# Optimization experiments

Measured on AMD Instinct MI355X. Metric: run time of the kernel, lower is better.

## Reference

```python
import jax, jax.numpy as jnp
import numpy as np

B, T, H, NSPK = 8, 1024, 1024, 2
LN_EPS = 1e-5


def setup_inputs() -> dict:
    key = jax.random.key(0)
    ks = jax.random.split(key, 12)
    s = 1.0 / np.sqrt(H)
    return {
        "x": jax.random.normal(ks[0], (B, T, H), jnp.float32),
        "qmask": jax.random.uniform(ks[1], (B, T, NSPK), jnp.float32),
        "dia_len": jax.random.randint(ks[2], (B,), T // 2, T + 1),
        "wp": 8,
        "wf": 8,
        "W_msg": jax.random.normal(ks[3], (H, H), jnp.float32) * s,
        "b_msg": jax.random.normal(ks[4], (H,), jnp.float32) * s,
        "W_self": jax.random.normal(ks[5], (H, H), jnp.float32) * s,
        "b_self": jax.random.normal(ks[6], (H,), jnp.float32) * s,
        "W_out": jax.random.normal(ks[7], (H, H), jnp.float32) * s,
        "b_out": jax.random.normal(ks[8], (H,), jnp.float32) * s,
        "gamma": jnp.ones((H,), jnp.float32),
        "beta": jnp.zeros((H,), jnp.float32),
    }


def reference(x, qmask, dia_len, wp, wf, W_msg, b_msg, W_self, b_self, W_out, b_out, gamma, beta):
    Bb, Tt, Hh = x.shape
    spk = jnp.argmax(qmask, axis=-1)                     # [B,T]
    pos = jnp.arange(Tt)
    offs = jnp.arange(-wp, wf + 1)                       # [W]
    idx = pos[:, None] + offs[None, :]                   # [T,W] window indices
    vlen = dia_len[:, None, None]                        # [B,1,1]
    valid = (idx[None] >= 0) & (idx[None] <= vlen - 1)   # [B,T,W]
    idxc = jnp.clip(idx, 0, Tt - 1)
    nb = jnp.take(x, idxc, axis=1)                       # [B,T,W,H]
    nb_spk = jnp.take(spk, idxc, axis=1)                 # [B,T,W]
    same = (nb_spk == spk[:, :, None]).astype(x.dtype)
    w = jnp.where(valid, 0.5 + 0.5 * same, 0.0)          # speaker weights, masked
    cnt = jnp.maximum(valid.sum(-1).astype(x.dtype), 1.0)  # window sizes [B,T]
    msg = jnp.einsum('btw,btwh->bth', w, nb) / cnt[..., None]
    h = x @ W_self + b_self + msg @ W_msg + b_msg        # per-node fusion
    node_valid = (pos[None, :] < dia_len[:, None])[..., None]
    out = jnp.where(node_valid, h, x)                    # nodes past dia_len keep x
    y = jax.nn.relu(out) @ W_out + b_out                 # dropout = identity (eval)
    z = x + y
    mean = z.mean(-1, keepdims=True)
    var = z.var(-1, keepdims=True)
    return gamma * (z - mean) / jnp.sqrt(var + LN_EPS) + beta
```

## Files before the change

### kernel.cpp

```cpp
#include <hip/hip_runtime.h>


typedef unsigned short u16;
typedef float floatx4 __attribute__((ext_vector_type(4)));
typedef short shortx8 __attribute__((ext_vector_type(8)));

#define T_ 1024
#define H_ 1024

__device__ __forceinline__ float bf2f(u16 v) {
    return __uint_as_float(((unsigned)v) << 16);
}
__device__ __forceinline__ u16 f2bf(float f) {
    unsigned u = __float_as_uint(f);
    return (u16)((u + 0x7fffu + ((u >> 16) & 1u)) >> 16);
}
__device__ __forceinline__ void async16(const void* g, void* l) {
    __builtin_amdgcn_global_load_lds(
        (__attribute__((address_space(1))) void*)g,
        (__attribute__((address_space(3))) void*)l, 16, 0, 0);
}

__global__ __launch_bounds__(256)
void pack_x(const float* __restrict__ x, u16* __restrict__ xbf)
{
    const size_t i = ((size_t)blockIdx.x * 256 + threadIdx.x) * 4;
    float4 v = *(const float4*)(x + i);
    ushort4 o;
    o.x = f2bf(v.x); o.y = f2bf(v.y); o.z = f2bf(v.z); o.w = f2bf(v.w);
    *(ushort4*)(xbf + i) = o;
}

__global__ __launch_bounds__(256)
void transpose_pack(const float* __restrict__ Wself, const float* __restrict__ Wmsg,
                    const float* __restrict__ Wout,
                    u16* __restrict__ wt1, u16* __restrict__ wt_out)
{
    __shared__ float s[32][33];
    const int wid = blockIdx.z;
    const float* src = (wid == 0) ? Wself : ((wid == 1) ? Wmsg : Wout);
    const int n0 = blockIdx.x * 32, k0 = blockIdx.y * 32;
    const int tx = threadIdx.x & 31, ty = threadIdx.x >> 5;
#pragma unroll
    for (int i = 0; i < 4; ++i) {
        int k = k0 + ty + 8 * i;
        s[ty + 8 * i][tx] = src[(size_t)k * H_ + n0 + tx];
    }
    __syncthreads();
#pragma unroll
    for (int i = 0; i < 4; ++i) {
        int n = n0 + ty + 8 * i;
        u16 v = f2bf(s[tx][ty + 8 * i]);
        if (wid == 0)      wt1[(size_t)n * 1024 + k0 + tx] = v;
        else if (wid == 1) wt1[(size_t)(n + 1024) * 1024 + k0 + tx] = v;
        else               wt_out[(size_t)n * 1024 + k0 + tx] = v;
    }
}

template <int KLEN, int EPI>
__global__ __launch_bounds__(256)
void gemm_bt(const u16* __restrict__ A, const u16* __restrict__ Bt,
             u16* __restrict__ O0, u16* __restrict__ O1)
{
    __shared__ u16 smem[2 * 8192];
    const int tid = threadIdx.x;
    const int bn = blockIdx.x * 128;
    const int bm = blockIdx.y * 128;
    const int kb = blockIdx.z * KLEN;
    const int wave = tid >> 6, lane = tid & 63;
    const int wr = wave >> 1, wc = wave & 1;
    const int lrow = lane & 15, lq = lane >> 4;

    const u16* gA0 = A + (size_t)(bm + (tid >> 2)) * 1024 + kb + (tid & 3) * 8;
    const u16* gA1 = gA0 + (size_t)64 * 1024;
    const u16* gB0 = Bt + (size_t)(bn + (tid >> 2)) * 1024 + kb + (tid & 3) * 8;
    const u16* gB1 = gB0 + (size_t)64 * 1024;

    floatx4 acc[4][4];
#pragma unroll
    for (int i = 0; i < 4; ++i)
#pragma unroll
        for (int j = 0; j < 4; ++j)
            acc[i][j] = (floatx4){0.f, 0.f, 0.f, 0.f};

    const int aoff = (wr * 64 + lrow) * 32 + lq * 8;
    const int boff = 4096 + (wc * 64 + lrow) * 32 + lq * 8;

    auto issue = [&](int s, int p) {
        u16* base = smem + p * 8192 + wave * 512;
        const int k = s * 32;
        async16(gA0 + k, base);
        async16(gA1 + k, base + 2048);
        async16(gB0 + k, base + 4096);
        async16(gB1 + k, base + 4096 + 2048);
    };

    constexpr int NS = KLEN / 32;
    issue(0, 0);
#pragma unroll 2
    for (int s = 0; s < NS; ++s) {
        const int p = s & 1;
        if (s + 1 < NS) {
            issue(s + 1, p ^ 1);
            asm volatile("s_waitcnt vmcnt(4)" ::: "memory");
        } else {
            asm volatile("s_waitcnt vmcnt(0)" ::: "memory");
        }
        asm volatile("s_barrier" ::: "memory");
        const u16* pa = smem + p * 8192 + aoff;
        const u16* pb = smem + p * 8192 + boff;
        shortx8 av[4], bv[4];
#pragma unroll
        for (int i = 0; i < 4; ++i) av[i] = *(const shortx8*)(pa + i * 512);
#pragma unroll
        for (int j = 0; j < 4; ++j) bv[j] = *(const shortx8*)(pb + j * 512);
#pragma unroll
        for (int i = 0; i < 4; ++i)
#pragma unroll
            for (int j = 0; j < 4; ++j)
                acc[i][j] = __builtin_amdgcn_mfma_f32_16x16x32_bf16(
                    av[i], bv[j], acc[i][j], 0, 0, 0);
        asm volatile("s_barrier" ::: "memory");
    }

    u16* O;
    int cbase;
    if (EPI == 0) { O = (bn < 1024) ? O0 : O1; cbase = bn & 1023; }
    else          { O = blockIdx.z ? O1 : O0;  cbase = bn; }
#pragma unroll
    for (int i = 0; i < 4; ++i) {
        const int row0 = bm + wr * 64 + i * 16 + lq * 4;
#pragma unroll
        for (int j = 0; j < 4; ++j) {
            const int col = cbase + wc * 64 + j * 16 + lrow;
#pragma unroll
            for (int r = 0; r < 4; ++r)
                O[(size_t)(row0 + r) * 1024 + col] = f2bf(acc[i][j][r]);
        }
    }
}

__global__ __launch_bounds__(256)
void combine(u16* uv, const u16* __restrict__ v,
             const float* __restrict__ x, const float* __restrict__ qmask,
             const int* __restrict__ dia_len, const float* __restrict__ b_self,
             const float* __restrict__ b_msg)
{
    __shared__ u16 sv[32][1024];
    const int tid = threadIdx.x;
    const int b = blockIdx.y;
    const int t0 = blockIdx.x * 16;
    const int dlen = dia_len[b];
    const int c4 = tid * 4;

    unsigned spkmask = 0;
#pragma unroll 4
    for (int rr = 0; rr < 32; ++rr) {
        int row = t0 - 8 + rr;
        row = row < 0 ? 0 : (row > T_ - 1 ? T_ - 1 : row);
        const float* q = qmask + ((size_t)b * T_ + row) * 2;
        spkmask |= (q[1] > q[0] ? 1u : 0u) << rr;
        *(ushort4*)&sv[rr][c4] =
            *(const ushort4*)(v + ((size_t)b * T_ + row) * 1024 + c4);
    }
    __syncthreads();

    float4 bs;
    {
        float4 b1 = *(const float4*)(b_self + c4);
        float4 b2 = *(const float4*)(b_msg + c4);
        bs.x = b1.x + b2.x; bs.y = b1.y + b2.y;
        bs.z = b1.z + b2.z; bs.w = b1.w + b2.w;
    }

    for (int lt = 0; lt < 16; ++lt) {
        const int t = t0 + lt;
        const unsigned cs = (spkmask >> (lt + 8)) & 1u;
        float a0 = 0.f, a1 = 0.f, a2 = 0.f, a3 = 0.f;
        int cnt = 0;
#pragma unroll
        for (int o = 0; o < 17; ++o) {
            const int idx = t + o - 8;
            if (idx >= 0 && idx < dlen) {
                const float w = (((spkmask >> (lt + o)) & 1u) == cs) ? 1.0f : 0.5f;
                ++cnt;
                ushort4 uu = *(const ushort4*)&sv[lt + o][c4];
                a0 += w * bf2f(uu.x); a1 += w * bf2f(uu.y);
                a2 += w * bf2f(uu.z); a3 += w * bf2f(uu.w);
            }
        }
        const float inv = 1.0f / (float)(cnt > 0 ? cnt : 1);
        const size_t rowg = (size_t)b * T_ + t;
        ushort4 u4 = *(const ushort4*)(uv + rowg * 1024 + c4);
        float4 xv = *(const float4*)(x + rowg * H_ + c4);
        const bool sel = (t < dlen);
        float h0 = bf2f(u4.x) + bs.x + a0 * inv;
        float h1 = bf2f(u4.y) + bs.y + a1 * inv;
        float h2 = bf2f(u4.z) + bs.z + a2 * inv;
        float h3 = bf2f(u4.w) + bs.w + a3 * inv;
        ushort4 outv;
        outv.x = f2bf(fmaxf(sel ? h0 : xv.x, 0.f));
        outv.y = f2bf(fmaxf(sel ? h1 : xv.y, 0.f));
        outv.z = f2bf(fmaxf(sel ? h2 : xv.z, 0.f));
        outv.w = f2bf(fmaxf(sel ? h3 : xv.w, 0.f));
        *(ushort4*)(uv + rowg * 1024 + c4) = outv;
    }
}

__global__ __launch_bounds__(256)
void ln_final(const u16* __restrict__ P0, const u16* __restrict__ P1,
              const float* __restrict__ x, const float* __restrict__ b_out,
              const float* __restrict__ gamma, const float* __restrict__ beta,
              float* __restrict__ out)
{
    const int row = blockIdx.x;
    const int tid = threadIdx.x;
    const size_t base = (size_t)row * H_ + tid * 4;
    float4 xv = *(const float4*)(x + base);
    ushort4 p0 = *(const ushort4*)(P0 + base);
    ushort4 p1 = *(const ushort4*)(P1 + base);
    float4 bo = *(const float4*)(b_out + tid * 4);
    float4 v;
    v.x = xv.x + bf2f(p0.x) + bf2f(p1.x) + bo.x;
    v.y = xv.y + bf2f(p0.y) + bf2f(p1.y) + bo.y;
    v.z = xv.z + bf2f(p0.z) + bf2f(p1.z) + bo.z;
    v.w = xv.w + bf2f(p0.w) + bf2f(p1.w) + bo.w;
    float s = v.x + v.y + v.z + v.w;
    float q = v.x * v.x + v.y * v.y + v.z * v.z + v.w * v.w;
#pragma unroll
    for (int off = 32; off > 0; off >>= 1) {
        s += __shfl_down(s, off);
        q += __shfl_down(q, off);
    }
    __shared__ float ps[4], pq[4];
    const int wave = tid >> 6, lane = tid & 63;
    if (lane == 0) { ps[wave] = s; pq[wave] = q; }
    __syncthreads();
    const float S = ps[0] + ps[1] + ps[2] + ps[3];
    const float Q = pq[0] + pq[1] + pq[2] + pq[3];
    const float mean = S * (1.0f / 1024.0f);
    const float var = Q * (1.0f / 1024.0f) - mean * mean;
    const float inv = rsqrtf(var + 1e-5f);
    float4 g = *(const float4*)(gamma + tid * 4);
    float4 bt = *(const float4*)(beta + tid * 4);
    float4 o;
    o.x = g.x * (v.x - mean) * inv + bt.x;
    o.y = g.y * (v.y - mean) * inv + bt.y;
    o.z = g.z * (v.z - mean) * inv + bt.z;
    o.w = g.w * (v.w - mean) * inv + bt.w;
    *(float4*)(out + base) = o;
}

extern "C" void kernel_launch(void* const* d_in, const int* in_sizes, int n_in,
                              void* d_out, int out_size, void* d_ws, size_t ws_size,
                              hipStream_t stream)
{
    (void)in_sizes; (void)n_in; (void)out_size; (void)ws_size;
    const float* x       = (const float*)d_in[0];
    const float* qmask   = (const float*)d_in[1];
    const int*   dia_len = (const int*)d_in[2];
    const float* W_msg   = (const float*)d_in[5];
    const float* b_msg   = (const float*)d_in[6];
    const float* W_self  = (const float*)d_in[7];
    const float* b_self  = (const float*)d_in[8];
    const float* W_out   = (const float*)d_in[9];
    const float* b_out   = (const float*)d_in[10];
    const float* gamma   = (const float*)d_in[11];
    const float* beta    = (const float*)d_in[12];
    float* out = (float*)d_out;

    char* ws = (char*)d_ws;
    u16* region0 = (u16*)ws;
    u16* region1 = (u16*)(ws + (size_t)(16u << 20));
    u16* region2 = (u16*)(ws + (size_t)(32u << 20));
    u16* wt1     = (u16*)(ws + (size_t)(48u << 20));
    u16* wt_out  = (u16*)(ws + (size_t)(52u << 20));

    pack_x<<<dim3(8192), 256, 0, stream>>>(x, region0);
    transpose_pack<<<dim3(32, 32, 3), 256, 0, stream>>>(W_self, W_msg, W_out,
                                                        wt1, wt_out);
    gemm_bt<1024, 0><<<dim3(16, 64, 1), 256, 0, stream>>>(region0, wt1,
                                                          region1, region2);
    combine<<<dim3(64, 8), 256, 0, stream>>>(region1, region2, x, qmask,
                                             dia_len, b_self, b_msg);
    gemm_bt<512, 1><<<dim3(8, 64, 2), 256, 0, stream>>>(region1, wt_out,
                                                        region2, region0);
    ln_final<<<dim3(8192), 256, 0, stream>>>(region2, region0, x, b_out,
                                             gamma, beta, out);
}
```

Measured before the change: 234.5 us.

## Merge prep kernels, load GEMM B operand directly to registers, simplify combine

Fuses the x bf16 pack and weight transpose into a single prep launch to cut one launch. The GEMM now loads B fragments straight from global memory into double-buffered registers instead of staging them through LDS, which halves shared memory and removes the LDS reads for B. The cost is uncoalesced per-lane global loads with no reuse across waves. The combine kernel becomes one row per block, reading the 17 neighbour rows from global/L2 instead of staging a 32-row tile in shared memory. That removes LDS pressure but raises global traffic roughly 17x for v.

```diff
diff --git a/kernel.cpp b/kernel.cpp
--- a/kernel.cpp
+++ b/kernel.cpp
@@ -22,38 +22,41 @@
 }
 
 __global__ __launch_bounds__(256)
-void pack_x(const float* __restrict__ x, u16* __restrict__ xbf)
-{
-    const size_t i = ((size_t)blockIdx.x * 256 + threadIdx.x) * 4;
-    float4 v = *(const float4*)(x + i);
-    ushort4 o;
-    o.x = f2bf(v.x); o.y = f2bf(v.y); o.z = f2bf(v.z); o.w = f2bf(v.w);
-    *(ushort4*)(xbf + i) = o;
-}
-
-__global__ __launch_bounds__(256)
-void transpose_pack(const float* __restrict__ Wself, const float* __restrict__ Wmsg,
-                    const float* __restrict__ Wout,
-                    u16* __restrict__ wt1, u16* __restrict__ wt_out)
+void prep(const float* __restrict__ Wself, const float* __restrict__ Wmsg,
+          const float* __restrict__ Wout, const float* __restrict__ x,
+          u16* __restrict__ wt1, u16* __restrict__ wt_out, u16* __restrict__ xbf)
 {
     __shared__ float s[32][33];
-    const int wid = blockIdx.z;
-    const float* src = (wid == 0) ? Wself : ((wid == 1) ? Wmsg : Wout);
-    const int n0 = blockIdx.x * 32, k0 = blockIdx.y * 32;
-    const int tx = threadIdx.x & 31, ty = threadIdx.x >> 5;
-#pragma unroll
-    for (int i = 0; i < 4; ++i) {
-        int k = k0 + ty + 8 * i;
-        s[ty + 8 * i][tx] = src[(size_t)k * H_ + n0 + tx];
-    }
-    __syncthreads();
-#pragma unroll
-    for (int i = 0; i < 4; ++i) {
-        int n = n0 + ty + 8 * i;
-        u16 v = f2bf(s[tx][ty + 8 * i]);
-        if (wid == 0)      wt1[(size_t)n * 1024 + k0 + tx] = v;
-        else if (wid == 1) wt1[(size_t)(n + 1024) * 1024 + k0 + tx] = v;
-        else               wt_out[(size_t)n * 1024 + k0 + tx] = v;
+    const int bid = blockIdx.x;
+    if (bid < 3072) {
+        const int wid = bid >> 10;
+        const int rem = bid & 1023;
+        const float* src = (wid == 0) ? Wself : ((wid == 1) ? Wmsg : Wout);
+        const int n0 = (rem & 31) * 32, k0 = (rem >> 5) * 32;
+        const int tx = threadIdx.x & 31, ty = threadIdx.x >> 5;
+#pragma unroll
+        for (int i = 0; i < 4; ++i) {
+            int k = k0 + ty + 8 * i;
+            s[ty + 8 * i][tx] = src[(size_t)k * H_ + n0 + tx];
+        }
+        __syncthreads();
+#pragma unroll
+        for (int i = 0; i < 4; ++i) {
+            int n = n0 + ty + 8 * i;
+            u16 v = f2bf(s[tx][ty + 8 * i]);
+            if (wid == 0)      wt1[(size_t)n * 1024 + k0 + tx] = v;
+            else if (wid == 1) wt1[(size_t)(n + 1024) * 1024 + k0 + tx] = v;
+            else               wt_out[(size_t)n * 1024 + k0 + tx] = v;
+        }
+    } else {
+        const size_t i = ((size_t)(bid - 3072) * 256 + threadIdx.x) * 8;
+        float4 v0 = *(const float4*)(x + i);
+        float4 v1 = *(const float4*)(x + i + 4);
+        ushort4 o0, o1;
+        o0.x = f2bf(v0.x); o0.y = f2bf(v0.y); o0.z = f2bf(v0.z); o0.w = f2bf(v0.w);
+        o1.x = f2bf(v1.x); o1.y = f2bf(v1.y); o1.z = f2bf(v1.z); o1.w = f2bf(v1.w);
+        *(ushort4*)(xbf + i) = o0;
+        *(ushort4*)(xbf + i + 4) = o1;
     }
 }
 
@@ -62,7 +65,7 @@
 void gemm_bt(const u16* __restrict__ A, const u16* __restrict__ Bt,
              u16* __restrict__ O0, u16* __restrict__ O1)
 {
-    __shared__ u16 smem[2 * 8192];
+    __shared__ u16 sA[2][4096];
     const int tid = threadIdx.x;
     const int bn = blockIdx.x * 128;
     const int bm = blockIdx.y * 128;
@@ -73,8 +76,7 @@
 
     const u16* gA0 = A + (size_t)(bm + (tid >> 2)) * 1024 + kb + (tid & 3) * 8;
     const u16* gA1 = gA0 + (size_t)64 * 1024;
-    const u16* gB0 = Bt + (size_t)(bn + (tid >> 2)) * 1024 + kb + (tid & 3) * 8;
-    const u16* gB1 = gB0 + (size_t)64 * 1024;
+    const u16* gB = Bt + (size_t)(bn + wc * 64 + lrow) * 1024 + kb + lq * 8;
 
     floatx4 acc[4][4];
 #pragma unroll
@@ -84,42 +86,45 @@
             acc[i][j] = (floatx4){0.f, 0.f, 0.f, 0.f};
 
     const int aoff = (wr * 64 + lrow) * 32 + lq * 8;
-    const int boff = 4096 + (wc * 64 + lrow) * 32 + lq * 8;
-
-    auto issue = [&](int s, int p) {
-        u16* base = smem + p * 8192 + wave * 512;
-        const int k = s * 32;
-        async16(gA0 + k, base);
-        async16(gA1 + k, base + 2048);
-        async16(gB0 + k, base + 4096);
-        async16(gB1 + k, base + 4096 + 2048);
-    };
 
     constexpr int NS = KLEN / 32;
-    issue(0, 0);
+    shortx8 breg[2][4];
+
+    {
+        u16* base = &sA[0][wave * 512];
+        async16(gA0, base);
+        async16(gA1, base + 2048);
+#pragma unroll
+        for (int j = 0; j < 4; ++j)
+            breg[0][j] = *(const shortx8*)(gB + (size_t)j * 16384);
+    }
+
 #pragma unroll 2
     for (int s = 0; s < NS; ++s) {
         const int p = s & 1;
         if (s + 1 < NS) {
-            issue(s + 1, p ^ 1);
-            asm volatile("s_waitcnt vmcnt(4)" ::: "memory");
+            u16* base = &sA[p ^ 1][wave * 512];
+            async16(gA0 + (s + 1) * 32, base);
+            async16(gA1 + (s + 1) * 32, base + 2048);
+#pragma unroll
+            for (int j = 0; j < 4; ++j)
+                breg[(s + 1) & 1][j] =
+                    *(const shortx8*)(gB + (size_t)j * 16384 + (s + 1) * 32);
+            asm volatile("s_waitcnt vmcnt(6)" ::: "memory");
         } else {
             asm volatile("s_waitcnt vmcnt(0)" ::: "memory");
         }
         asm volatile("s_barrier" ::: "memory");
-        const u16* pa = smem + p * 8192 + aoff;
-        const u16* pb = smem + p * 8192 + boff;
-        shortx8 av[4], bv[4];
+        const u16* pa = &sA[p][aoff];
+        shortx8 av[4];
 #pragma unroll
         for (int i = 0; i < 4; ++i) av[i] = *(const shortx8*)(pa + i * 512);
-#pragma unroll
-        for (int j = 0; j < 4; ++j) bv[j] = *(const shortx8*)(pb + j * 512);
 #pragma unroll
         for (int i = 0; i < 4; ++i)
 #pragma unroll
             for (int j = 0; j < 4; ++j)
                 acc[i][j] = __builtin_amdgcn_mfma_f32_16x16x32_bf16(
-                    av[i], bv[j], acc[i][j], 0, 0, 0);
+                    av[i], breg[s & 1][j], acc[i][j], 0, 0, 0);
         asm volatile("s_barrier" ::: "memory");
     }
 
@@ -141,29 +146,46 @@
 }
 
 __global__ __launch_bounds__(256)
-void combine(u16* uv, const u16* __restrict__ v,
+void combine(u16* __restrict__ uv, const u16* __restrict__ v,
              const float* __restrict__ x, const float* __restrict__ qmask,
              const int* __restrict__ dia_len, const float* __restrict__ b_self,
              const float* __restrict__ b_msg)
 {
-    __shared__ u16 sv[32][1024];
+    const int t = blockIdx.x;
+    const int b = blockIdx.y;
     const int tid = threadIdx.x;
-    const int b = blockIdx.y;
-    const int t0 = blockIdx.x * 16;
     const int dlen = dia_len[b];
     const int c4 = tid * 4;
-
-    unsigned spkmask = 0;
-#pragma unroll 4
-    for (int rr = 0; rr < 32; ++rr) {
-        int row = t0 - 8 + rr;
-        row = row < 0 ? 0 : (row > T_ - 1 ? T_ - 1 : row);
-        const float* q = qmask + ((size_t)b * T_ + row) * 2;
-        spkmask |= (q[1] > q[0] ? 1u : 0u) << rr;
-        *(ushort4*)&sv[rr][c4] =
-            *(const ushort4*)(v + ((size_t)b * T_ + row) * 1024 + c4);
-    }
-    __syncthreads();
+    const size_t rowg = (size_t)b * T_ + t;
+
+    const float* qb = qmask + (size_t)b * T_ * 2;
+    const int spk_t = (qb[t * 2 + 1] > qb[t * 2]) ? 1 : 0;
+
+    float wts[17];
+    int cnt = 0;
+#pragma unroll
+    for (int o = 0; o < 17; ++o) {
+        const int idx = t + o - 8;
+        if (idx >= 0 && idx < dlen) {
+            ++cnt;
+            const int spk_i = (qb[idx * 2 + 1] > qb[idx * 2]) ? 1 : 0;
+            wts[o] = (spk_i == spk_t) ? 1.0f : 0.5f;
+        } else {
+            wts[o] = 0.0f;
+        }
+    }
+    const float inv = 1.0f / (float)(cnt > 0 ? cnt : 1);
+
+    float a0 = 0.f, a1 = 0.f, a2 = 0.f, a3 = 0.f;
+#pragma unroll
+    for (int o = 0; o < 17; ++o) {
+        if (wts[o] != 0.0f) {
+            const float w = wts[o] * inv;
+            ushort4 vv = *(const ushort4*)(v + (rowg + (o - 8)) * 1024 + c4);
+            a0 += w * bf2f(vv.x); a1 += w * bf2f(vv.y);
+            a2 += w * bf2f(vv.z); a3 += w * bf2f(vv.w);
+        }
+    }
 
     float4 bs;
     {
@@ -173,38 +195,19 @@
         bs.z = b1.z + b2.z; bs.w = b1.w + b2.w;
     }
 
-    for (int lt = 0; lt < 16; ++lt) {
-        const int t = t0 + lt;
-        const unsigned cs = (spkmask >> (lt + 8)) & 1u;
-        float a0 = 0.f, a1 = 0.f, a2 = 0.f, a3 = 0.f;
-        int cnt = 0;
-#pragma unroll
-        for (int o = 0; o < 17; ++o) {
-            const int idx = t + o - 8;
-            if (idx >= 0 && idx < dlen) {
-                const float w = (((spkmask >> (lt + o)) & 1u) == cs) ? 1.0f : 0.5f;
-                ++cnt;
-                ushort4 uu = *(const ushort4*)&sv[lt + o][c4];
-                a0 += w * bf2f(uu.x); a1 += w * bf2f(uu.y);
-                a2 += w * bf2f(uu.z); a3 += w * bf2f(uu.w);
-            }
-        }
-        const float inv = 1.0f / (float)(cnt > 0 ? cnt : 1);
-        const size_t rowg = (size_t)b * T_ + t;
-        ushort4 u4 = *(const ushort4*)(uv + rowg * 1024 + c4);
-        float4 xv = *(const float4*)(x + rowg * H_ + c4);
-        const bool sel = (t < dlen);
-        float h0 = bf2f(u4.x) + bs.x + a0 * inv;
-        float h1 = bf2f(u4.y) + bs.y + a1 * inv;
-        float h2 = bf2f(u4.z) + bs.z + a2 * inv;
-        float h3 = bf2f(u4.w) + bs.w + a3 * inv;
-        ushort4 outv;
-        outv.x = f2bf(fmaxf(sel ? h0 : xv.x, 0.f));
-        outv.y = f2bf(fmaxf(sel ? h1 : xv.y, 0.f));
-        outv.z = f2bf(fmaxf(sel ? h2 : xv.z, 0.f));
-        outv.w = f2bf(fmaxf(sel ? h3 : xv.w, 0.f));
-        *(ushort4*)(uv + rowg * 1024 + c4) = outv;
-    }
+    ushort4 u4 = *(const ushort4*)(uv + rowg * 1024 + c4);
+    float4 xv = *(const float4*)(x + rowg * H_ + c4);
+    const bool sel = (t < dlen);
+    float h0 = bf2f(u4.x) + bs.x + a0;
+    float h1 = bf2f(u4.y) + bs.y + a1;
+    float h2 = bf2f(u4.z) + bs.z + a2;
+    float h3 = bf2f(u4.w) + bs.w + a3;
+    ushort4 outv;
+    outv.x = f2bf(fmaxf(sel ? h0 : xv.x, 0.f));
+    outv.y = f2bf(fmaxf(sel ? h1 : xv.y, 0.f));
+    outv.z = f2bf(fmaxf(sel ? h2 : xv.z, 0.f));
+    outv.w = f2bf(fmaxf(sel ? h3 : xv.w, 0.f));
+    *(ushort4*)(uv + rowg * 1024 + c4) = outv;
 }
 
 __global__ __launch_bounds__(256)
@@ -276,12 +279,11 @@
     u16* wt1     = (u16*)(ws + (size_t)(48u << 20));
     u16* wt_out  = (u16*)(ws + (size_t)(52u << 20));
 
-    pack_x<<<dim3(8192), 256, 0, stream>>>(x, region0);
-    transpose_pack<<<dim3(32, 32, 3), 256, 0, stream>>>(W_self, W_msg, W_out,
-                                                        wt1, wt_out);
+    prep<<<dim3(7168), 256, 0, stream>>>(W_self, W_msg, W_out, x,
+                                         wt1, wt_out, region0);
     gemm_bt<1024, 0><<<dim3(16, 64, 1), 256, 0, stream>>>(region0, wt1,
                                                           region1, region2);
-    combine<<<dim3(64, 8), 256, 0, stream>>>(region1, region2, x, qmask,
+    combine<<<dim3(T_, 8), 256, 0, stream>>>(region1, region2, x, qmask,
                                              dia_len, b_self, b_msg);
     gemm_bt<512, 1><<<dim3(8, 64, 2), 256, 0, stream>>>(region1, wt_out,
                                                         region2, region0);
```

Result: slower. 282.7 us (+20.6%).
